# Performance work log

Measured on AMD Instinct MI355X. Metric: run time of the kernel, lower is better.

The kernel has to match this reference:

```python
import jax, jax.numpy as jnp
import numpy as np

B, T, D, H, L, C = 64, 512, 256, 1024, 2, 128


def setup_inputs() -> dict:
    key = jax.random.key(0)
    ks = jax.random.split(key, 11)
    s = 0.05
    return {
        "x": jax.random.normal(ks[0], (B, T, D), dtype=jnp.float32),
        "W_ih0": jax.random.normal(ks[1], (4 * H, D), dtype=jnp.float32) * s,
        "W_hh0": jax.random.normal(ks[2], (4 * H, H), dtype=jnp.float32) * s,
        "b_ih0": jax.random.normal(ks[3], (4 * H,), dtype=jnp.float32) * s,
        "b_hh0": jax.random.normal(ks[4], (4 * H,), dtype=jnp.float32) * s,
        "W_ih1": jax.random.normal(ks[5], (4 * H, H), dtype=jnp.float32) * s,
        "W_hh1": jax.random.normal(ks[6], (4 * H, H), dtype=jnp.float32) * s,
        "b_ih1": jax.random.normal(ks[7], (4 * H,), dtype=jnp.float32) * s,
        "b_hh1": jax.random.normal(ks[8], (4 * H,), dtype=jnp.float32) * s,
        "W_fc": jax.random.normal(ks[9], (C, H), dtype=jnp.float32) * s,
        "b_fc": jax.random.normal(ks[10], (C,), dtype=jnp.float32) * s,
    }


def _lstm_cell(inp, h, c, Wi, Wh, bi, bh):
    # PyTorch LSTMCell: gates ordered i, f, g, o
    gates = inp @ Wi.T + bi + h @ Wh.T + bh  # [B, 4H]
    i, f, g, o = jnp.split(gates, 4, axis=-1)
    c_new = jax.nn.sigmoid(f) * c + jax.nn.sigmoid(i) * jnp.tanh(g)
    h_new = jax.nn.sigmoid(o) * jnp.tanh(c_new)
    return h_new, c_new


def reference(x, W_ih0, W_hh0, b_ih0, b_hh0, W_ih1, W_hh1, b_ih1, b_hh1, W_fc, b_fc):
    b = x.shape[0]
    h0 = jnp.zeros((b, H), x.dtype)
    init = (h0, h0, h0, h0)  # (h_l0, c_l0, h_l1, c_l1)

    def step(carry, x_t):
        h0_, c0_, h1_, c1_ = carry
        h0n, c0n = _lstm_cell(x_t, h0_, c0_, W_ih0, W_hh0, b_ih0, b_hh0)
        h1n, c1n = _lstm_cell(h0n, h1_, c1_, W_ih1, W_hh1, b_ih1, b_hh1)
        return (h0n, c0n, h1n, c1n), None

    xt = jnp.swapaxes(x, 0, 1)  # [T, B, D]
    (h0f, c0f, h1f, c1f), _ = jax.lax.scan(step, init, xt)
    return h1f @ W_fc.T + b_fc  # [B, num_classes]
```

## Files before the change

### kernel.cpp

```cpp
#include <hip/hip_runtime.h>
#include <hip/hip_bf16.h>

#define B_ 64
#define T_ 512
#define D_ 256
#define H_ 1024
#define RING 64
#define PS 260

typedef __attribute__((ext_vector_type(8))) short short8;
typedef __attribute__((ext_vector_type(4))) float floatx4;

__device__ __forceinline__ unsigned short f2bf(float f){
  unsigned u = __builtin_bit_cast(unsigned, f);
  u = (u + 0x7fffu + ((u >> 16) & 1u)) >> 16;
  return (unsigned short)u;
}

__device__ __forceinline__ short8 pack8(floatx4 a, floatx4 b){
  short8 r;
  r[0]=(short)f2bf(a[0]); r[1]=(short)f2bf(a[1]); r[2]=(short)f2bf(a[2]); r[3]=(short)f2bf(a[3]);
  r[4]=(short)f2bf(b[0]); r[5]=(short)f2bf(b[1]); r[6]=(short)f2bf(b[2]); r[7]=(short)f2bf(b[3]);
  return r;
}

__device__ __forceinline__ float sigm(float v){ return 1.f/(1.f+__expf(-v)); }
__device__ __forceinline__ float tanh_f(float v){ return 1.f - 2.f/(1.f+__expf(2.f*v)); }

__device__ __forceinline__ void gpoll(const unsigned long long* watch,
                                      unsigned& seen0, unsigned& seen1,
                                      unsigned tgt0, unsigned tgt1){
  if (__all(seen0 >= tgt0 && seen1 >= tgt1)) return;
  long g = 0;
  for (;;){
    unsigned long long v = __hip_atomic_load(watch, __ATOMIC_RELAXED, __HIP_MEMORY_SCOPE_AGENT);
    unsigned v0 = (unsigned)v, v1 = (unsigned)(v >> 32);
    seen0 = v0 > seen0 ? v0 : seen0;
    seen1 = v1 > seen1 ? v1 : seen1;
    if (__all(seen0 >= tgt0 && seen1 >= tgt1)) break;
    if (++g > (1L<<24)) break;
  }
}

template<int LAYER>
__device__ __forceinline__ void run_lstm(
    const float* __restrict__ x,
    const float* __restrict__ Wi, const float* __restrict__ Wh,
    const float* __restrict__ bi, const float* __restrict__ bh,
    unsigned* seq, unsigned short* h0h, unsigned short* h1h, float* h1f,
    int jbase, int j, int half,
    float* partial , float* c_st , float* biasv )
{
  constexpr int NK = LAYER ? 8 : 5;
  constexpr int KA = LAYER ? 1024 : 256;

  const int tid  = threadIdx.x;
  const int wave = tid >> 6;
  const int lane = tid & 63;
  const int n15  = lane & 15;
  const int kq   = (lane >> 4) * 8;

  short8 bfr[4][NK];
  #pragma unroll
  for (int nt = 0; nt < 4; nt++){
    int n   = nt*16 + n15;
    int row = (n >> 4)*H_ + jbase + (n & 15);
    #pragma unroll
    for (int ks = 0; ks < NK; ks++){
      int k = (LAYER ? (ks < 4 ? 1024 + wave*128 + ks*32 : wave*128 + (ks-4)*32)
                     : (ks == 0 ? wave*32 : 256 + wave*128 + (ks-1)*32)) + kq;
      const float* s = (k < KA) ? (Wi + (size_t)row*KA + k)
                                : (Wh + (size_t)row*H_ + (k - KA));
      bfr[nt][ks] = pack8(*(const floatx4*)s, *(const floatx4*)(s + 4));
    }
  }
  if (tid < 64){
    int col = (tid >> 4)*H_ + jbase + (tid & 15);
    biasv[tid] = bi[col] + bh[col];
  }
  c_st[tid & 511] = 0.f;
  __syncthreads();

  const unsigned long long* watch =
      (const unsigned long long*)seq + (size_t)(half*64 + wave*8 + (lane & 7));

  unsigned seen0 = 0, seen1 = 0;
  unsigned long long vf = 0;

  for (int t = 0; t < T_; t++){
    { unsigned p0 = (unsigned)vf, p1 = (unsigned)(vf >> 32);
      seen0 = p0 > seen0 ? p0 : seen0;
      seen1 = p1 > seen1 ? p1 : seen1; }

    floatx4 xr[2][2];
    if constexpr (LAYER == 0){
      #pragma unroll
      for (int mt = 0; mt < 2; mt++){
        const float* xs = x + ((size_t)(half*32 + mt*16 + n15)*T_ + t)*D_ + wave*32 + kq;
        xr[mt][0] = *(const floatx4*)xs;
        xr[mt][1] = *(const floatx4*)(xs + 4);
      }
    }

    floatx4 acc[2][4];
    #pragma unroll
    for (int mt = 0; mt < 2; mt++)
      #pragma unroll
      for (int nt = 0; nt < 4; nt++)
        acc[mt][nt] = (floatx4)0.f;

    const unsigned short* h0t = h0h + ((size_t)((LAYER ? t : (t-1)) & (RING-1)) << 16);
    const unsigned short* h1t = h1h + ((size_t)((t-1) & (RING-1)) << 16);

    if constexpr (LAYER == 0){
      {
        short8 afr0 = pack8(xr[0][0], xr[0][1]);
        short8 afr1 = pack8(xr[1][0], xr[1][1]);
        #pragma unroll
        for (int nt = 0; nt < 4; nt++){
          acc[0][nt] = __builtin_amdgcn_mfma_f32_16x16x32_bf16(afr0, bfr[nt][0], acc[0][nt], 0, 0, 0);
          acc[1][nt] = __builtin_amdgcn_mfma_f32_16x16x32_bf16(afr1, bfr[nt][0], acc[1][nt], 0, 0, 0);
        }
      }
      __builtin_amdgcn_sched_barrier(0);
      gpoll(watch, seen0, seen1, (unsigned)t,
            (t >= RING) ? (unsigned)(t - RING + 1) : 0u);
      __builtin_amdgcn_sched_barrier(0);
      if (t > 0){
        #pragma unroll
        for (int ks = 1; ks < 5; ks++){
          const int hk = wave*128 + (ks-1)*32 + kq;
          const unsigned short* p = h0t + ((hk >> 4) << 10) + (hk & 15);
          short8 afr[2];
          #pragma unroll
          for (int mt = 0; mt < 2; mt++)
            afr[mt] = *(const short8*)(p + ((half*32 + mt*16 + n15) << 4));
          #pragma unroll
          for (int mt = 0; mt < 2; mt++)
            #pragma unroll
            for (int nt = 0; nt < 4; nt++)
              acc[mt][nt] = __builtin_amdgcn_mfma_f32_16x16x32_bf16(afr[mt], bfr[nt][ks], acc[mt][nt], 0, 0, 0);
        }
      }
    } else {
      gpoll(watch, seen0, seen1, 0u, (unsigned)t);
      __builtin_amdgcn_sched_barrier(0);
      if (t > 0){
        #pragma unroll
        for (int ks = 0; ks < 4; ks++){
          const int hk = wave*128 + ks*32 + kq;
          const unsigned short* p = h1t + ((hk >> 4) << 10) + (hk & 15);
          short8 afr[2];
          #pragma unroll
          for (int mt = 0; mt < 2; mt++)
            afr[mt] = *(const short8*)(p + ((half*32 + mt*16 + n15) << 4));
          #pragma unroll
          for (int mt = 0; mt < 2; mt++)
            #pragma unroll
            for (int nt = 0; nt < 4; nt++)
              acc[mt][nt] = __builtin_amdgcn_mfma_f32_16x16x32_bf16(afr[mt], bfr[nt][ks], acc[mt][nt], 0, 0, 0);
        }
      }
      __builtin_amdgcn_sched_barrier(0);
      gpoll(watch, seen0, seen1, (unsigned)(t + 1), 0u);
      __builtin_amdgcn_sched_barrier(0);
      #pragma unroll
      for (int ks = 4; ks < 8; ks++){
        const int hk = wave*128 + (ks-4)*32 + kq;
        const unsigned short* p = h0t + ((hk >> 4) << 10) + (hk & 15);
        short8 afr[2];
        #pragma unroll
        for (int mt = 0; mt < 2; mt++)
          afr[mt] = *(const short8*)(p + ((half*32 + mt*16 + n15) << 4));
        #pragma unroll
        for (int mt = 0; mt < 2; mt++)
          #pragma unroll
          for (int nt = 0; nt < 4; nt++)
            acc[mt][nt] = __builtin_amdgcn_mfma_f32_16x16x32_bf16(afr[mt], bfr[nt][ks], acc[mt][nt], 0, 0, 0);
      }
    }

    #pragma unroll
    for (int mt = 0; mt < 2; mt++)
      #pragma unroll
      for (int nt = 0; nt < 4; nt++){
        int n  = nt*16 + n15;
        int b0 = mt*16 + (lane >> 4)*4;
        *(floatx4*)(partial + (size_t)n*PS + wave*32 + b0) = acc[mt][nt];
      }
    __syncthreads();

    {
      int b = tid >> 4, jj = tid & 15;
      float g[4];
      #pragma unroll
      for (int q = 0; q < 4; q++){
        const float* p = partial + (size_t)(q*16 + jj)*PS + b;
        float s = biasv[q*16 + jj];
        #pragma unroll
        for (int ss = 0; ss < 8; ss++) s += p[ss*32];
        g[q] = s;
      }
      float co = c_st[tid];
      float si = sigm(g[0]), sf = sigm(g[1]), tg = tanh_f(g[2]), so = sigm(g[3]);
      float cn = sf*co + si*tg;
      float hn = so*tanh_f(cn);
      c_st[tid] = cn;
      unsigned hb = (unsigned)f2bf(hn);
      unsigned ob = (unsigned)__shfl_xor((int)hb, 1, 64);
      if (!(jj & 1)){
        unsigned pk = hb | (ob << 16);
        unsigned short* dst = (LAYER ? h1h : h0h)
                            + ((size_t)(t & (RING-1)) << 16)
                            + ((size_t)j << 10) + ((size_t)(half*32 + b) << 4) + jj;
        __hip_atomic_store((unsigned*)dst, pk, __ATOMIC_RELAXED, __HIP_MEMORY_SCOPE_AGENT);
      }
      if (LAYER == 1 && t == T_-1)
        h1f[(size_t)(half*32 + b)*H_ + jbase + jj] = hn;
    }
    vf = __hip_atomic_load(watch, __ATOMIC_RELAXED, __HIP_MEMORY_SCOPE_AGENT);
    __syncthreads();
    if (tid == 0)
      __hip_atomic_store(seq + (size_t)(half*64 + j)*2 + LAYER, (unsigned)(t + 1),
                         __ATOMIC_RELAXED, __HIP_MEMORY_SCOPE_AGENT);
  }
}

__global__ __launch_bounds__(512, 2) void lstm_pk(
    const float* __restrict__ x,
    const float* __restrict__ Wih0, const float* __restrict__ Whh0,
    const float* __restrict__ bih0, const float* __restrict__ bhh0,
    const float* __restrict__ Wih1, const float* __restrict__ Whh1,
    const float* __restrict__ bih1, const float* __restrict__ bhh1,
    char* __restrict__ ws)
{
  __shared__ __align__(16) float partial[64*PS];
  __shared__ float c_st[512];
  __shared__ float biasv[64];

  unsigned* seq       = (unsigned*)ws;
  unsigned short* h0h = (unsigned short*)(ws + (1<<20));
  unsigned short* h1h = (unsigned short*)(ws + (1<<20) + RING*B_*H_*2);
  float* h1f          = (float*)(ws + (1<<20) + 2*(size_t)RING*B_*H_*2);

  const int bid = blockIdx.x;
  if (bid < 128){
    run_lstm<0>(x, Wih0, Whh0, bih0, bhh0, seq, h0h, h1h, h1f,
                (bid & 63)*16, bid & 63, bid >> 6, partial, c_st, biasv);
  } else {
    const int r = bid - 128;
    run_lstm<1>(x, Wih1, Whh1, bih1, bhh1, seq, h0h, h1h, h1f,
                (r & 63)*16, r & 63, r >> 6, partial, c_st, biasv);
  }
}

__global__ __launch_bounds__(128) void fc_k(
    const float* __restrict__ h1f, const float* __restrict__ Wfc,
    const float* __restrict__ bfc, float* __restrict__ out)
{
  __shared__ float hv[1024];
  int b = blockIdx.x, c = threadIdx.x;
  for (int i = c; i < 1024; i += 128) hv[i] = h1f[(size_t)b*1024 + i];
  __syncthreads();
  const floatx4* w4 = (const floatx4*)(Wfc + (size_t)c*1024);
  const floatx4* h4 = (const floatx4*)hv;
  float acc = 0.f;
  #pragma unroll 8
  for (int k = 0; k < 256; k++){
    floatx4 wv = w4[k];
    floatx4 hh = h4[k];
    acc += wv[0]*hh[0] + wv[1]*hh[1] + wv[2]*hh[2] + wv[3]*hh[3];
  }
  out[(size_t)b*128 + c] = acc + bfc[c];
}

extern "C" void kernel_launch(void* const* d_in, const int* in_sizes, int n_in,
                              void* d_out, int out_size, void* d_ws, size_t ws_size,
                              hipStream_t stream)
{
  const float* x    = (const float*)d_in[0];
  const float* Wih0 = (const float*)d_in[1];
  const float* Whh0 = (const float*)d_in[2];
  const float* bih0 = (const float*)d_in[3];
  const float* bhh0 = (const float*)d_in[4];
  const float* Wih1 = (const float*)d_in[5];
  const float* Whh1 = (const float*)d_in[6];
  const float* bih1 = (const float*)d_in[7];
  const float* bhh1 = (const float*)d_in[8];
  const float* Wfc  = (const float*)d_in[9];
  const float* bfc  = (const float*)d_in[10];

  hipMemsetAsync(d_ws, 0, 4096, stream);

  lstm_pk<<<256, 512, 0, stream>>>(x, Wih0, Whh0, bih0, bhh0, Wih1, Whh1, bih1, bhh1, (char*)d_ws);

  const float* h1f = (const float*)((char*)d_ws + (1<<20) + 2*(size_t)RING*B_*H_*2);
  fc_k<<<64, 128, 0, stream>>>(h1f, Wfc, bfc, (float*)d_out);
}
```

Baseline: 3.472 ms.

## Delegate global flag polling to one wave per block and broadcast readiness via LDS

Instead of every wave polling the global sequence flags across the device, only one or two designated waves per block poll (each lane watches one producer), then publish readiness through a shared-memory flag that the other waves spin on. Layer 0's K split is also redistributed so each wave covers a contiguous 160-wide slice spanning x and h, loading x inline. This is meant to cut global atomic polling traffic and latency on the per-step cross-block barrier. It adds an extra intra-block handoff hop and uneven per-wave work in layer 0.

```diff
diff --git a/kernel.cpp b/kernel.cpp
--- a/kernel.cpp
+++ b/kernel.cpp
@@ -42,6 +42,13 @@
   }
 }
 
+__device__ __forceinline__ void lspin(unsigned* flag, unsigned tgt){
+  long g = 0;
+  while (__hip_atomic_load(flag, __ATOMIC_RELAXED, __HIP_MEMORY_SCOPE_WORKGROUP) < tgt){
+    if (++g > (1L<<24)) break;
+  }
+}
+
 template<int LAYER>
 __device__ __forceinline__ void run_lstm(
     const float* __restrict__ x,
@@ -49,7 +56,8 @@
     const float* __restrict__ bi, const float* __restrict__ bh,
     unsigned* seq, unsigned short* h0h, unsigned short* h1h, float* h1f,
     int jbase, int j, int half,
-    float* partial , float* c_st , float* biasv )
+    float* partial , float* c_st , float* biasv ,
+    unsigned* rdy )
 {
   constexpr int NK = LAYER ? 8 : 5;
   constexpr int KA = LAYER ? 1024 : 256;
@@ -68,7 +76,7 @@
     #pragma unroll
     for (int ks = 0; ks < NK; ks++){
       int k = (LAYER ? (ks < 4 ? 1024 + wave*128 + ks*32 : wave*128 + (ks-4)*32)
-                     : (ks == 0 ? wave*32 : 256 + wave*128 + (ks-1)*32)) + kq;
+                     : wave*160 + ks*32) + kq;
       const float* s = (k < KA) ? (Wi + (size_t)row*KA + k)
                                 : (Wh + (size_t)row*H_ + (k - KA));
       bfr[nt][ks] = pack8(*(const floatx4*)s, *(const floatx4*)(s + 4));
@@ -79,10 +87,12 @@
     biasv[tid] = bi[col] + bh[col];
   }
   c_st[tid & 511] = 0.f;
+  if (tid == 0){ rdy[0] = 0u; rdy[1] = 0u; }
   __syncthreads();
 
   const unsigned long long* watch =
-      (const unsigned long long*)seq + (size_t)(half*64 + wave*8 + (lane & 7));
+      (const unsigned long long*)seq + (size_t)(half*64 + lane);
+  const bool isPoll = LAYER ? (wave == 0 || wave == 4) : (wave <= 1);
 
   unsigned seen0 = 0, seen1 = 0;
   unsigned long long vf = 0;
@@ -92,16 +102,6 @@
       seen0 = p0 > seen0 ? p0 : seen0;
       seen1 = p1 > seen1 ? p1 : seen1; }
 
-    floatx4 xr[2][2];
-    if constexpr (LAYER == 0){
-      #pragma unroll
-      for (int mt = 0; mt < 2; mt++){
-        const float* xs = x + ((size_t)(half*32 + mt*16 + n15)*T_ + t)*D_ + wave*32 + kq;
-        xr[mt][0] = *(const floatx4*)xs;
-        xr[mt][1] = *(const floatx4*)(xs + 4);
-      }
-    }
-
     floatx4 acc[2][4];
     #pragma unroll
     for (int mt = 0; mt < 2; mt++)
@@ -113,28 +113,17 @@
     const unsigned short* h1t = h1h + ((size_t)((t-1) & (RING-1)) << 16);
 
     if constexpr (LAYER == 0){
-      {
-        short8 afr0 = pack8(xr[0][0], xr[0][1]);
-        short8 afr1 = pack8(xr[1][0], xr[1][1]);
-        #pragma unroll
-        for (int nt = 0; nt < 4; nt++){
-          acc[0][nt] = __builtin_amdgcn_mfma_f32_16x16x32_bf16(afr0, bfr[nt][0], acc[0][nt], 0, 0, 0);
-          acc[1][nt] = __builtin_amdgcn_mfma_f32_16x16x32_bf16(afr1, bfr[nt][0], acc[1][nt], 0, 0, 0);
-        }
-      }
-      __builtin_amdgcn_sched_barrier(0);
-      gpoll(watch, seen0, seen1, (unsigned)t,
-            (t >= RING) ? (unsigned)(t - RING + 1) : 0u);
-      __builtin_amdgcn_sched_barrier(0);
-      if (t > 0){
-        #pragma unroll
-        for (int ks = 1; ks < 5; ks++){
-          const int hk = wave*128 + (ks-1)*32 + kq;
-          const unsigned short* p = h0t + ((hk >> 4) << 10) + (hk & 15);
+      #pragma unroll
+      for (int ks = 0; ks < NK; ks++){
+        const int kb = wave*160 + ks*32;
+        if (kb < D_){
+          const int kk = kb + kq;
           short8 afr[2];
           #pragma unroll
-          for (int mt = 0; mt < 2; mt++)
-            afr[mt] = *(const short8*)(p + ((half*32 + mt*16 + n15) << 4));
+          for (int mt = 0; mt < 2; mt++){
+            const float* xs = x + ((size_t)(half*32 + mt*16 + n15)*T_ + t)*D_ + kk;
+            afr[mt] = pack8(*(const floatx4*)xs, *(const floatx4*)(xs + 4));
+          }
           #pragma unroll
           for (int mt = 0; mt < 2; mt++)
             #pragma unroll
@@ -142,8 +131,44 @@
               acc[mt][nt] = __builtin_amdgcn_mfma_f32_16x16x32_bf16(afr[mt], bfr[nt][ks], acc[mt][nt], 0, 0, 0);
         }
       }
+      __builtin_amdgcn_sched_barrier(0);
+      if (wave == 0){
+        gpoll(watch, seen0, seen1, 0u, (t >= RING) ? (unsigned)(t - RING + 1) : 0u);
+      } else if (wave == 1){
+        gpoll(watch, seen0, seen1, (unsigned)t, 0u);
+        if (lane == 0) __hip_atomic_store(&rdy[0], (unsigned)(t + 1),
+                                          __ATOMIC_RELAXED, __HIP_MEMORY_SCOPE_WORKGROUP);
+      } else {
+        lspin(&rdy[0], (unsigned)(t + 1));
+      }
+      __builtin_amdgcn_sched_barrier(0);
+      if (t > 0){
+        #pragma unroll
+        for (int ks = 0; ks < NK; ks++){
+          const int kb = wave*160 + ks*32;
+          if (kb >= D_){
+            const int hk = kb - D_ + kq;
+            const unsigned short* p = h0t + ((hk >> 4) << 10) + (hk & 15);
+            short8 afr[2];
+            #pragma unroll
+            for (int mt = 0; mt < 2; mt++)
+              afr[mt] = *(const short8*)(p + ((half*32 + mt*16 + n15) << 4));
+            #pragma unroll
+            for (int mt = 0; mt < 2; mt++)
+              #pragma unroll
+              for (int nt = 0; nt < 4; nt++)
+                acc[mt][nt] = __builtin_amdgcn_mfma_f32_16x16x32_bf16(afr[mt], bfr[nt][ks], acc[mt][nt], 0, 0, 0);
+          }
+        }
+      }
     } else {
-      gpoll(watch, seen0, seen1, 0u, (unsigned)t);
+      if (wave == 4){
+        gpoll(watch, seen0, seen1, 0u, (unsigned)t);
+        if (lane == 0) __hip_atomic_store(&rdy[1], (unsigned)(t + 1),
+                                          __ATOMIC_RELAXED, __HIP_MEMORY_SCOPE_WORKGROUP);
+      } else {
+        lspin(&rdy[1], (unsigned)(t + 1));
+      }
       __builtin_amdgcn_sched_barrier(0);
       if (t > 0){
         #pragma unroll
@@ -162,7 +187,13 @@
         }
       }
       __builtin_amdgcn_sched_barrier(0);
-      gpoll(watch, seen0, seen1, (unsigned)(t + 1), 0u);
+      if (wave == 0){
+        gpoll(watch, seen0, seen1, (unsigned)(t + 1), 0u);
+        if (lane == 0) __hip_atomic_store(&rdy[0], (unsigned)(t + 1),
+                                          __ATOMIC_RELAXED, __HIP_MEMORY_SCOPE_WORKGROUP);
+      } else {
+        lspin(&rdy[0], (unsigned)(t + 1));
+      }
       __builtin_amdgcn_sched_barrier(0);
       #pragma unroll
       for (int ks = 4; ks < 8; ks++){
@@ -218,7 +249,8 @@
       if (LAYER == 1 && t == T_-1)
         h1f[(size_t)(half*32 + b)*H_ + jbase + jj] = hn;
     }
-    vf = __hip_atomic_load(watch, __ATOMIC_RELAXED, __HIP_MEMORY_SCOPE_AGENT);
+    if (isPoll)
+      vf = __hip_atomic_load(watch, __ATOMIC_RELAXED, __HIP_MEMORY_SCOPE_AGENT);
     __syncthreads();
     if (tid == 0)
       __hip_atomic_store(seq + (size_t)(half*64 + j)*2 + LAYER, (unsigned)(t + 1),
@@ -237,6 +269,7 @@
   __shared__ __align__(16) float partial[64*PS];
   __shared__ float c_st[512];
   __shared__ float biasv[64];
+  __shared__ unsigned rdy[2];
 
   unsigned* seq       = (unsigned*)ws;
   unsigned short* h0h = (unsigned short*)(ws + (1<<20));
@@ -246,11 +279,11 @@
   const int bid = blockIdx.x;
   if (bid < 128){
     run_lstm<0>(x, Wih0, Whh0, bih0, bhh0, seq, h0h, h1h, h1f,
-                (bid & 63)*16, bid & 63, bid >> 6, partial, c_st, biasv);
+                (bid & 63)*16, bid & 63, bid >> 6, partial, c_st, biasv, rdy);
   } else {
     const int r = bid - 128;
     run_lstm<1>(x, Wih1, Whh1, bih1, bhh1, seq, h0h, h1h, h1f,
-                (r & 63)*16, r & 63, r >> 6, partial, c_st, biasv);
+                (r & 63)*16, r & 63, r >> 6, partial, c_st, biasv, rdy);
   }
 }
 
```

New measurement: 3.507 ms. About the same (+1.0%).
